# Performance work log

Measured on AMD Instinct MI355X. Metric: run time of the kernel, lower is better.

Reference implementation:

```python
import jax, jax.numpy as jnp
import numpy as np

B, N, D = 2, 2048, 2048
H, I, K, V = 16, 1, 128, 128
EPS = 1e-6


def setup_inputs() -> dict:
    key = jax.random.key(0)
    ks = jax.random.split(key, 6)
    x_q = jax.random.normal(ks[0], (B, N, D), dtype=jnp.float32)
    # norm_mask: lower-triangular causal mask (the 'nm' operand); values in [0,1]
    norm_mask = jnp.tril(jax.random.uniform(ks[1], (N, N), dtype=jnp.float32))
    scale = 1.0 / np.sqrt(D)
    w_q = jax.random.normal(ks[2], (D, H, I, K), dtype=jnp.float32) * scale
    w_k = jax.random.normal(ks[3], (D, H, K), dtype=jnp.float32) * scale
    w_v = jax.random.normal(ks[4], (D, H, V), dtype=jnp.float32) * scale
    w_o = jax.random.normal(ks[5], (H, I, V, D), dtype=jnp.float32) * (1.0 / np.sqrt(H * I * V))
    rms_scale = jnp.ones((V,), dtype=jnp.float32)
    return {"x_q": x_q, "norm_mask": norm_mask, "w_q": w_q, "w_k": w_k,
            "w_v": w_v, "rms_scale": rms_scale, "w_o": w_o}


def reference(x_q, norm_mask, w_q, w_k, w_v, rms_scale, w_o):
    # self-attention: x_k = x_v = x_q
    q = jnp.einsum('bnd,dhik->bnhik', x_q, w_q)   # (B,N,H,I,K)
    k = jnp.einsum('bnd,dhk->bnhk', x_q, w_k)     # (B,N,H,K)
    v = jnp.einsum('bnd,dhv->bnhv', x_q, w_v)     # (B,N,H,V)
    # linear (no-softmax) attention with decay/normalization mask 'nm'
    s = jnp.einsum('bnhik,bmhk->bnhim', q, k)     # (B,N,H,I,N)
    s = s * norm_mask[None, :, None, None, :]
    y = jnp.einsum('bnhim,bmhv->bnhiv', s, v)     # (B,N,H,I,V)
    # RMSNorm over v_head_d
    ms = jnp.mean(jnp.square(y), axis=-1, keepdims=True)
    y = y * jax.lax.rsqrt(ms + EPS) * rms_scale
    # output projection
    return jnp.einsum('bnhiv,hivd->bnd', y, w_o)
```

## Files before the change

### kernel.cpp

```cpp
#include <hip/hip_runtime.h>
#include <hip/hip_bf16.h>


typedef _Float16 f16x8 __attribute__((ext_vector_type(8)));
typedef _Float16 f16x4 __attribute__((ext_vector_type(4)));
typedef float    f32x4 __attribute__((ext_vector_type(4)));

#define DEV static __device__ __forceinline__

DEV int swzx(int row) { return (((row & 7) ^ ((row >> 3) & 7)) << 4); }

typedef const unsigned int __attribute__((address_space(1)))* gas_t;
typedef unsigned int __attribute__((address_space(3)))* las_t;
DEV void gld16(const void* g, void* l) {
  __builtin_amdgcn_global_load_lds((gas_t)g, (las_t)l, 16, 0, 0);
}

__global__ void k_cast_h(const float* __restrict__ in, _Float16* __restrict__ out, int n) {
  int i = (blockIdx.x * blockDim.x + threadIdx.x) * 4;
  int stride = gridDim.x * blockDim.x * 4;
  for (; i < n; i += stride) {
    float4 v = *reinterpret_cast<const float4*>(in + i);
    f16x4 o;
    o[0] = (_Float16)v.x; o[1] = (_Float16)v.y;
    o[2] = (_Float16)v.z; o[3] = (_Float16)v.w;
    *reinterpret_cast<f16x4*>(out + i) = o;
  }
}

__global__ void k_transpose_h(const float* __restrict__ in, _Float16* __restrict__ out) {
  __shared__ float tile[32][33];
  int tx = threadIdx.x, ty = threadIdx.y;
  int c0 = blockIdx.x * 32, r0 = blockIdx.y * 32;
  #pragma unroll
  for (int j = 0; j < 4; ++j)
    tile[ty + j * 8][tx] = in[(size_t)(r0 + ty + j * 8) * 2048 + c0 + tx];
  __syncthreads();
  #pragma unroll
  for (int j = 0; j < 4; ++j)
    out[(size_t)(c0 + ty + j * 8) * 2048 + r0 + tx] = (_Float16)tile[tx][ty + j * 8];
}

__global__ void k_transpose_v(const _Float16* __restrict__ in, _Float16* __restrict__ out) {
  __shared__ _Float16 tile[32][33];
  int tx = threadIdx.x, ty = threadIdx.y;
  int v0 = blockIdx.x * 32, n0 = blockIdx.y * 32, bh = blockIdx.z;
  int b = bh >> 4, h = bh & 15;
  #pragma unroll
  for (int j = 0; j < 4; ++j)
    tile[ty + j * 8][tx] =
        in[((size_t)(b * 2048 + n0 + ty + j * 8) * 16 + h) * 128 + v0 + tx];
  __syncthreads();
  #pragma unroll
  for (int j = 0; j < 4; ++j)
    out[((size_t)bh * 128 + v0 + ty + j * 8) * 2048 + n0 + tx] = tile[tx][ty + j * 8];
}

template <int OUTF32>
__global__ __launch_bounds__(256) void k_gemm1(const _Float16* __restrict__ A,
                                               const _Float16* __restrict__ B,
                                               void* __restrict__ C) {
  __shared__ __align__(16) _Float16 As[128 * 64];
  __shared__ __align__(16) _Float16 Bs[128 * 64];
  const int tid = threadIdx.x;
  const int lane = tid & 63, w = tid >> 6;
  const int lr = lane & 15, lg = lane >> 4;
  const int bm = blockIdx.y, bn = blockIdx.x;
  const int wr = (w >> 1) * 64, wc = (w & 1) * 64;

  f32x4 acc[4][4];
  #pragma unroll
  for (int i = 0; i < 4; ++i)
    #pragma unroll
    for (int j = 0; j < 4; ++j) { f32x4 z = {0.f, 0.f, 0.f, 0.f}; acc[i][j] = z; }

  const size_t aOff = (size_t)(bm * 128) * 2048;
  const size_t bOff = (size_t)(bn * 128) * 2048;

  for (int kt = 0; kt < 32; ++kt) {
    __syncthreads();
    #pragma unroll
    for (int it = 0; it < 4; ++it) {
      int row = it * 32 + (tid >> 3);
      int cb  = ((tid & 7) * 16) ^ swzx(row);
      size_t g = (size_t)row * 2048 + kt * 64 + (cb >> 1);
      int ld = it * 4096 + tid * 16;
      gld16(A + aOff + g, (char*)As + ld);
      gld16(B + bOff + g, (char*)Bs + ld);
    }
    __syncthreads();
    #pragma unroll
    for (int ks = 0; ks < 2; ++ks) {
      f16x8 af[4], bf[4];
      #pragma unroll
      for (int f = 0; f < 4; ++f) {
        int ar = wr + f * 16 + lr;
        af[f] = *reinterpret_cast<const f16x8*>((const char*)As + ar * 128 +
                                                ((ks * 64 + lg * 16) ^ swzx(ar)));
        int br = wc + f * 16 + lr;
        bf[f] = *reinterpret_cast<const f16x8*>((const char*)Bs + br * 128 +
                                                ((ks * 64 + lg * 16) ^ swzx(br)));
      }
      #pragma unroll
      for (int i = 0; i < 4; ++i)
        #pragma unroll
        for (int j = 0; j < 4; ++j)
          acc[i][j] = __builtin_amdgcn_mfma_f32_16x16x32_f16(af[i], bf[j], acc[i][j], 0, 0, 0);
    }
  }

  #pragma unroll
  for (int fm = 0; fm < 4; ++fm)
    #pragma unroll
    for (int fn = 0; fn < 4; ++fn)
      #pragma unroll
      for (int r = 0; r < 4; ++r) {
        int grow = bm * 128 + wr + fm * 16 + lg * 4 + r;
        int gcol = bn * 128 + wc + fn * 16 + lr;
        float v = acc[fm][fn][r];
        size_t o = (size_t)grow * 2048 + gcol;
        if (OUTF32) ((float*)C)[o] = v;
        else        ((_Float16*)C)[o] = (_Float16)v;
      }
}

__global__ __launch_bounds__(512) void k_attn1(const _Float16* __restrict__ qv,
                                               const _Float16* __restrict__ kv,
                                               const _Float16* __restrict__ vt,
                                               const float* __restrict__ nm,
                                               const float* __restrict__ rms_scale,
                                               _Float16* __restrict__ y) {
  __shared__ __align__(16) _Float16 Ks[2][64 * 128];
  __shared__ __align__(16) _Float16 Vs[2][128 * 64];
  __shared__ __align__(16) _Float16 Ps[128 * 64];
  const int tid = threadIdx.x;
  const int lane = tid & 63, w = tid >> 6;
  const int lr = lane & 15, lg = lane >> 4;
  const int bh = blockIdx.x, b = bh >> 4, h = bh & 15;
  const size_t base  = (size_t)b * 2048 * 2048 + (size_t)h * 128;
  const size_t vbase = (size_t)bh * 128 * 2048;

  const int krow = tid >> 4, kc = tid & 15;
  const int vrow = tid >> 3, vc = tid & 7;

  auto STAGE = [&](int t, int bufi) {
    #pragma unroll
    for (int it = 0; it < 2; ++it) {
      int kr = it * 32 + krow;
      int gk = ((kc * 16) ^ swzx(kr)) >> 1;
      gld16(kv + base + (size_t)(t * 64 + kr) * 2048 + gk,
            (char*)Ks[bufi] + it * 8192 + tid * 16);
      int vr = it * 64 + vrow;
      int gv = ((vc * 16) ^ swzx(vr)) >> 1;
      gld16(vt + vbase + (size_t)vr * 2048 + t * 64 + gv,
            (char*)Vs[bufi] + it * 8192 + tid * 16);
    }
  };

  #pragma unroll
  for (int pi = 0; pi < 2; ++pi) {
    const int qt = pi ? (15 - (int)blockIdx.y) : (int)blockIdx.y;
    const int nT = 2 * qt + 2;

    f16x8 aq[4];
    {
      size_t qrow = base + (size_t)(qt * 128 + w * 16 + lr) * 2048;
      #pragma unroll
      for (int ks = 0; ks < 4; ++ks)
        aq[ks] = *reinterpret_cast<const f16x8*>(qv + qrow + ks * 32 + lg * 8);
    }

    f32x4 accY[8];
    #pragma unroll
    for (int i = 0; i < 8; ++i) { f32x4 z = {0.f, 0.f, 0.f, 0.f}; accY[i] = z; }

    STAGE(0, 0);
    asm volatile("s_waitcnt vmcnt(0)" ::: "memory");
    __builtin_amdgcn_s_barrier();
    __builtin_amdgcn_sched_barrier(0);

    for (int t = 0; t < nT; ++t) {
      const int cur = t & 1;

      float nmv[4][4];
      #pragma unroll
      for (int fm = 0; fm < 4; ++fm)
        #pragma unroll
        for (int r = 0; r < 4; ++r)
          nmv[fm][r] = nm[(size_t)(qt * 128 + w * 16 + lg * 4 + r) * 2048 +
                          t * 64 + fm * 16 + lr];
      __builtin_amdgcn_sched_barrier(0);

      if (t + 1 < nT) STAGE(t + 1, cur ^ 1);

      f32x4 accS[4];
      #pragma unroll
      for (int i = 0; i < 4; ++i) { f32x4 z = {0.f, 0.f, 0.f, 0.f}; accS[i] = z; }
      #pragma unroll
      for (int ks = 0; ks < 4; ++ks) {
        #pragma unroll
        for (int fm = 0; fm < 4; ++fm) {
          int br = fm * 16 + lr;
          f16x8 bk = *reinterpret_cast<const f16x8*>(
              (const char*)Ks[cur] + br * 256 + ((ks * 64 + lg * 16) ^ swzx(br)));
          accS[fm] = __builtin_amdgcn_mfma_f32_16x16x32_f16(aq[ks], bk, accS[fm], 0, 0, 0);
        }
      }

      #pragma unroll
      for (int fm = 0; fm < 4; ++fm)
        #pragma unroll
        for (int r = 0; r < 4; ++r) {
          float pv = accS[fm][r] * nmv[fm][r];
          int pr = w * 16 + lg * 4 + r, pc = fm * 16 + lr;
          *reinterpret_cast<_Float16*>((char*)Ps + pr * 128 + ((pc * 2) ^ swzx(pr))) =
              (_Float16)pv;
        }

      #pragma unroll
      for (int ks = 0; ks < 2; ++ks) {
        int ar = w * 16 + lr;
        f16x8 ap = *reinterpret_cast<const f16x8*>(
            (const char*)Ps + ar * 128 + ((ks * 64 + lg * 16) ^ swzx(ar)));
        #pragma unroll
        for (int fv = 0; fv < 8; ++fv) {
          int br = fv * 16 + lr;
          f16x8 bv = *reinterpret_cast<const f16x8*>(
              (const char*)Vs[cur] + br * 128 + ((ks * 64 + lg * 16) ^ swzx(br)));
          accY[fv] = __builtin_amdgcn_mfma_f32_16x16x32_f16(ap, bv, accY[fv], 0, 0, 0);
        }
      }

      asm volatile("s_waitcnt vmcnt(0)" ::: "memory");
      __builtin_amdgcn_s_barrier();
      __builtin_amdgcn_sched_barrier(0);
    }

    #pragma unroll
    for (int r = 0; r < 4; ++r) {
      float sq = 0.f;
      #pragma unroll
      for (int fv = 0; fv < 8; ++fv) { float yy = accY[fv][r]; sq += yy * yy; }
      sq += __shfl_xor(sq, 1); sq += __shfl_xor(sq, 2);
      sq += __shfl_xor(sq, 4); sq += __shfl_xor(sq, 8);
      float scale = rsqrtf(sq * (1.0f / 128.0f) + 1e-6f);
      int nrow = qt * 128 + w * 16 + lg * 4 + r;
      size_t orow = ((size_t)b * 2048 + nrow) * 2048 + (size_t)h * 128;
      #pragma unroll
      for (int fv = 0; fv < 8; ++fv) {
        int col = fv * 16 + lr;
        y[orow + col] = (_Float16)(accY[fv][r] * scale * rms_scale[col]);
      }
    }
  }
}

extern "C" void kernel_launch(void* const* d_in, const int* in_sizes, int n_in,
                              void* d_out, int out_size, void* d_ws, size_t ws_size,
                              hipStream_t stream) {
  (void)in_sizes; (void)n_in; (void)out_size; (void)ws_size;
  const float* x  = (const float*)d_in[0];
  const float* nm = (const float*)d_in[1];
  const float* wq = (const float*)d_in[2];
  const float* wk = (const float*)d_in[3];
  const float* wv = (const float*)d_in[4];
  const float* rs = (const float*)d_in[5];
  const float* wo = (const float*)d_in[6];

  _Float16* p = (_Float16*)d_ws;
  _Float16* xf  = p; p += 8388608;
  _Float16* wt  = p; p += 4194304;
  _Float16* qf  = p; p += 8388608;
  _Float16* kf  = p; p += 8388608;
  _Float16* vf  = p; p += 8388608;
  _Float16* vtf = p; p += 8388608;

  k_cast_h<<<dim3(2048), dim3(256), 0, stream>>>(x, xf, 8388608);

  k_transpose_h<<<dim3(64, 64), dim3(32, 8), 0, stream>>>(wq, wt);
  k_gemm1<0><<<dim3(16, 32), dim3(256), 0, stream>>>(xf, wt, qf);
  k_transpose_h<<<dim3(64, 64), dim3(32, 8), 0, stream>>>(wk, wt);
  k_gemm1<0><<<dim3(16, 32), dim3(256), 0, stream>>>(xf, wt, kf);
  k_transpose_h<<<dim3(64, 64), dim3(32, 8), 0, stream>>>(wv, wt);
  k_gemm1<0><<<dim3(16, 32), dim3(256), 0, stream>>>(xf, wt, vf);
  k_transpose_v<<<dim3(4, 64, 32), dim3(32, 8), 0, stream>>>(vf, vtf);
  k_transpose_h<<<dim3(64, 64), dim3(32, 8), 0, stream>>>(wo, wt);

  k_attn1<<<dim3(32, 8), dim3(512), 0, stream>>>(qf, kf, vtf, nm, rs, xf);

  k_gemm1<1><<<dim3(16, 32), dim3(256), 0, stream>>>(xf, wt, d_out);
}
```

Measured before the change: 299.0 us.

## Fuse QKV projections into one GEMM and shrink attention tiles to 64 rows

Transposes the Q, K and V weights into one contiguous 6144-wide matrix so a single GEMM launch with 1536 blocks writes an interleaved QKV buffer. The attention kernel now reads Q and K from that buffer with stride 6144. It also moves from 512-thread blocks over 128-query tiles to 256-thread blocks over 64-query tiles, doubling the grid for better occupancy and load balance. s_setprio is raised around the MFMA sections to favour matrix issue, at the cost of strided reads and more K/V restaging per query row.

```diff
diff --git a/kernel.cpp b/kernel.cpp
--- a/kernel.cpp
+++ b/kernel.cpp
@@ -49,7 +49,7 @@
   #pragma unroll
   for (int j = 0; j < 4; ++j)
     tile[ty + j * 8][tx] =
-        in[((size_t)(b * 2048 + n0 + ty + j * 8) * 16 + h) * 128 + v0 + tx];
+        in[(size_t)(b * 2048 + n0 + ty + j * 8) * 6144 + 4096 + h * 128 + v0 + tx];
   __syncthreads();
   #pragma unroll
   for (int j = 0; j < 4; ++j)
@@ -59,7 +59,7 @@
 template <int OUTF32>
 __global__ __launch_bounds__(256) void k_gemm1(const _Float16* __restrict__ A,
                                                const _Float16* __restrict__ B,
-                                               void* __restrict__ C) {
+                                               void* __restrict__ C, int ldc) {
   __shared__ __align__(16) _Float16 As[128 * 64];
   __shared__ __align__(16) _Float16 Bs[128 * 64];
   const int tid = threadIdx.x;
@@ -101,11 +101,13 @@
         bf[f] = *reinterpret_cast<const f16x8*>((const char*)Bs + br * 128 +
                                                 ((ks * 64 + lg * 16) ^ swzx(br)));
       }
+      __builtin_amdgcn_s_setprio(1);
       #pragma unroll
       for (int i = 0; i < 4; ++i)
         #pragma unroll
         for (int j = 0; j < 4; ++j)
           acc[i][j] = __builtin_amdgcn_mfma_f32_16x16x32_f16(af[i], bf[j], acc[i][j], 0, 0, 0);
+      __builtin_amdgcn_s_setprio(0);
     }
   }
 
@@ -118,26 +120,26 @@
         int grow = bm * 128 + wr + fm * 16 + lg * 4 + r;
         int gcol = bn * 128 + wc + fn * 16 + lr;
         float v = acc[fm][fn][r];
-        size_t o = (size_t)grow * 2048 + gcol;
+        size_t o = (size_t)grow * ldc + gcol;
         if (OUTF32) ((float*)C)[o] = v;
         else        ((_Float16*)C)[o] = (_Float16)v;
       }
 }
 
-__global__ __launch_bounds__(512) void k_attn1(const _Float16* __restrict__ qv,
-                                               const _Float16* __restrict__ kv,
+__global__ __launch_bounds__(256) void k_attn1(const _Float16* __restrict__ qkv,
                                                const _Float16* __restrict__ vt,
                                                const float* __restrict__ nm,
                                                const float* __restrict__ rms_scale,
                                                _Float16* __restrict__ y) {
   __shared__ __align__(16) _Float16 Ks[2][64 * 128];
   __shared__ __align__(16) _Float16 Vs[2][128 * 64];
-  __shared__ __align__(16) _Float16 Ps[128 * 64];
+  __shared__ __align__(16) _Float16 Ps[64 * 64];
   const int tid = threadIdx.x;
   const int lane = tid & 63, w = tid >> 6;
   const int lr = lane & 15, lg = lane >> 4;
   const int bh = blockIdx.x, b = bh >> 4, h = bh & 15;
-  const size_t base  = (size_t)b * 2048 * 2048 + (size_t)h * 128;
+  const _Float16* qb = qkv + (size_t)b * 2048 * 6144 + h * 128;
+  const _Float16* kb = qkv + (size_t)b * 2048 * 6144 + 2048 + h * 128;
   const size_t vbase = (size_t)bh * 128 * 2048;
 
   const int krow = tid >> 4, kc = tid & 15;
@@ -145,29 +147,29 @@
 
   auto STAGE = [&](int t, int bufi) {
     #pragma unroll
-    for (int it = 0; it < 2; ++it) {
-      int kr = it * 32 + krow;
+    for (int it = 0; it < 4; ++it) {
+      int kr = it * 16 + krow;
       int gk = ((kc * 16) ^ swzx(kr)) >> 1;
-      gld16(kv + base + (size_t)(t * 64 + kr) * 2048 + gk,
-            (char*)Ks[bufi] + it * 8192 + tid * 16);
-      int vr = it * 64 + vrow;
+      gld16(kb + (size_t)(t * 64 + kr) * 6144 + gk,
+            (char*)Ks[bufi] + it * 4096 + tid * 16);
+      int vr = it * 32 + vrow;
       int gv = ((vc * 16) ^ swzx(vr)) >> 1;
       gld16(vt + vbase + (size_t)vr * 2048 + t * 64 + gv,
-            (char*)Vs[bufi] + it * 8192 + tid * 16);
+            (char*)Vs[bufi] + it * 4096 + tid * 16);
     }
   };
 
   #pragma unroll
   for (int pi = 0; pi < 2; ++pi) {
-    const int qt = pi ? (15 - (int)blockIdx.y) : (int)blockIdx.y;
-    const int nT = 2 * qt + 2;
+    const int qt = pi ? (31 - (int)blockIdx.y) : (int)blockIdx.y;
+    const int nT = qt + 1;
 
     f16x8 aq[4];
     {
-      size_t qrow = base + (size_t)(qt * 128 + w * 16 + lr) * 2048;
+      const _Float16* qrow = qb + (size_t)(qt * 64 + w * 16 + lr) * 6144;
       #pragma unroll
       for (int ks = 0; ks < 4; ++ks)
-        aq[ks] = *reinterpret_cast<const f16x8*>(qv + qrow + ks * 32 + lg * 8);
+        aq[ks] = *reinterpret_cast<const f16x8*>(qrow + ks * 32 + lg * 8);
     }
 
     f32x4 accY[8];
@@ -187,7 +189,7 @@
       for (int fm = 0; fm < 4; ++fm)
         #pragma unroll
         for (int r = 0; r < 4; ++r)
-          nmv[fm][r] = nm[(size_t)(qt * 128 + w * 16 + lg * 4 + r) * 2048 +
+          nmv[fm][r] = nm[(size_t)(qt * 64 + w * 16 + lg * 4 + r) * 2048 +
                           t * 64 + fm * 16 + lr];
       __builtin_amdgcn_sched_barrier(0);
 
@@ -196,6 +198,7 @@
       f32x4 accS[4];
       #pragma unroll
       for (int i = 0; i < 4; ++i) { f32x4 z = {0.f, 0.f, 0.f, 0.f}; accS[i] = z; }
+      __builtin_amdgcn_s_setprio(1);
       #pragma unroll
       for (int ks = 0; ks < 4; ++ks) {
         #pragma unroll
@@ -206,6 +209,7 @@
           accS[fm] = __builtin_amdgcn_mfma_f32_16x16x32_f16(aq[ks], bk, accS[fm], 0, 0, 0);
         }
       }
+      __builtin_amdgcn_s_setprio(0);
 
       #pragma unroll
       for (int fm = 0; fm < 4; ++fm)
@@ -217,6 +221,7 @@
               (_Float16)pv;
         }
 
+      __builtin_amdgcn_s_setprio(1);
       #pragma unroll
       for (int ks = 0; ks < 2; ++ks) {
         int ar = w * 16 + lr;
@@ -230,6 +235,7 @@
           accY[fv] = __builtin_amdgcn_mfma_f32_16x16x32_f16(ap, bv, accY[fv], 0, 0, 0);
         }
       }
+      __builtin_amdgcn_s_setprio(0);
 
       asm volatile("s_waitcnt vmcnt(0)" ::: "memory");
       __builtin_amdgcn_s_barrier();
@@ -244,7 +250,7 @@
       sq += __shfl_xor(sq, 1); sq += __shfl_xor(sq, 2);
       sq += __shfl_xor(sq, 4); sq += __shfl_xor(sq, 8);
       float scale = rsqrtf(sq * (1.0f / 128.0f) + 1e-6f);
-      int nrow = qt * 128 + w * 16 + lg * 4 + r;
+      int nrow = qt * 64 + w * 16 + lg * 4 + r;
       size_t orow = ((size_t)b * 2048 + nrow) * 2048 + (size_t)h * 128;
       #pragma unroll
       for (int fv = 0; fv < 8; ++fv) {
@@ -269,24 +275,22 @@
 
   _Float16* p = (_Float16*)d_ws;
   _Float16* xf  = p; p += 8388608;
-  _Float16* wt  = p; p += 4194304;
-  _Float16* qf  = p; p += 8388608;
-  _Float16* kf  = p; p += 8388608;
-  _Float16* vf  = p; p += 8388608;
+  _Float16* wt3 = p; p += 12582912;
+  _Float16* wto = p; p += 4194304;
+  _Float16* qkv = p; p += 25165824;
   _Float16* vtf = p; p += 8388608;
 
   k_cast_h<<<dim3(2048), dim3(256), 0, stream>>>(x, xf, 8388608);
 
-  k_transpose_h<<<dim3(64, 64), dim3(32, 8), 0, stream>>>(wq, wt);
-  k_gemm1<0><<<dim3(16, 32), dim3(256), 0, stream>>>(xf, wt, qf);
-  k_transpose_h<<<dim3(64, 64), dim3(32, 8), 0, stream>>>(wk, wt);
-  k_gemm1<0><<<dim3(16, 32), dim3(256), 0, stream>>>(xf, wt, kf);
-  k_transpose_h<<<dim3(64, 64), dim3(32, 8), 0, stream>>>(wv, wt);
-  k_gemm1<0><<<dim3(16, 32), dim3(256), 0, stream>>>(xf, wt, vf);
-  k_transpose_v<<<dim3(4, 64, 32), dim3(32, 8), 0, stream>>>(vf, vtf);
-  k_transpose_h<<<dim3(64, 64), dim3(32, 8), 0, stream>>>(wo, wt);
-
-  k_attn1<<<dim3(32, 8), dim3(512), 0, stream>>>(qf, kf, vtf, nm, rs, xf);
-
-  k_gemm1<1><<<dim3(16, 32), dim3(256), 0, stream>>>(xf, wt, d_out);
-}
+  k_transpose_h<<<dim3(64, 64), dim3(32, 8), 0, stream>>>(wq, wt3);
+  k_transpose_h<<<dim3(64, 64), dim3(32, 8), 0, stream>>>(wk, wt3 + 4194304);
+  k_transpose_h<<<dim3(64, 64), dim3(32, 8), 0, stream>>>(wv, wt3 + 8388608);
+  k_transpose_h<<<dim3(64, 64), dim3(32, 8), 0, stream>>>(wo, wto);
+
+  k_gemm1<0><<<dim3(48, 32), dim3(256), 0, stream>>>(xf, wt3, qkv, 6144);
+  k_transpose_v<<<dim3(4, 64, 32), dim3(32, 8), 0, stream>>>(qkv, vtf);
+
+  k_attn1<<<dim3(32, 16), dim3(256), 0, stream>>>(qkv, vtf, nm, rs, xf);
+
+  k_gemm1<1><<<dim3(16, 32), dim3(256), 0, stream>>>(xf, wto, d_out, 2048);
+}
```

Measured after the change: 283.9 us. 5.1% less time.
